# Kernel tuning notes

Measured on AMD Instinct MI355X. Metric: run time of the kernel, lower is better.

Reference implementation:

```python
import math
import jax, jax.numpy as jnp
import numpy as np

D_MODEL = 2048
HEAD = 128
DEPTH = 12
LAMBDA_INIT = 0.8 - 0.6 * math.exp(-0.3 * DEPTH)
RMS_EPS = float(np.finfo(np.float32).eps)  # torch RMSNorm default eps=None -> finfo.eps


def setup_inputs() -> dict:
    key = jax.random.key(0)
    ks = jax.random.split(key, 9)
    B, S = 2, 4096
    std_l = 0.1
    return {
        "x": jax.random.normal(ks[0], (B, S, D_MODEL), dtype=jnp.float32),
        "Wq": jax.random.normal(ks[1], (HEAD, D_MODEL), dtype=jnp.float32) / math.sqrt(D_MODEL),
        "Wk": jax.random.normal(ks[2], (HEAD, D_MODEL), dtype=jnp.float32) / math.sqrt(D_MODEL),
        "Wv": jax.random.normal(ks[3], (HEAD, D_MODEL), dtype=jnp.float32) / math.sqrt(D_MODEL),
        "lambda_q1": std_l * jax.random.normal(ks[4], (HEAD // 2,), dtype=jnp.float32),
        "lambda_q2": std_l * jax.random.normal(ks[5], (HEAD // 2,), dtype=jnp.float32),
        "lambda_k1": std_l * jax.random.normal(ks[6], (HEAD // 2,), dtype=jnp.float32),
        "lambda_k2": std_l * jax.random.normal(ks[7], (HEAD // 2,), dtype=jnp.float32),
        "rms_weight": jnp.ones((HEAD,), dtype=jnp.float32),
    }


def reference(x, Wq, Wk, Wv, lambda_q1, lambda_q2, lambda_k1, lambda_k2, rms_weight):
    # projections (torch Linear: x @ W.T)
    q = jnp.einsum("bsd,hd->bsh", x, Wq)
    k = jnp.einsum("bsd,hd->bsh", x, Wk)
    v = jnp.einsum("bsd,hd->bsh", x, Wv)
    h2 = HEAD // 2
    q1, q2 = q[..., :h2], q[..., h2:]
    k1, k2 = k[..., :h2], k[..., h2:]
    scale = 1.0 / math.sqrt(h2)
    attn1 = jax.nn.softmax(jnp.einsum("bqh,bkh->bqk", q1, k1) * scale, axis=-1)
    attn2 = jax.nn.softmax(jnp.einsum("bqh,bkh->bqk", q2, k2) * scale, axis=-1)
    lam = jnp.exp(jnp.dot(lambda_q1, lambda_k1)) - jnp.exp(jnp.dot(lambda_q2, lambda_k2)) + LAMBDA_INIT
    attn_out = jnp.einsum("bqk,bkh->bqh", attn1 - lam * attn2, v)
    # RMSNorm over last dim
    rms = jax.lax.rsqrt(jnp.mean(attn_out * attn_out, axis=-1, keepdims=True) + RMS_EPS)
    return (1.0 - LAMBDA_INIT) * (attn_out * rms * rms_weight)
```

## Files before the change

kernel.cpp:

```cpp
#include <hip/hip_runtime.h>
#include <hip/hip_bf16.h>
#include <math.h>

#define S_LEN 4096
#define DMODEL 2048
#define HEADD 128

typedef __attribute__((ext_vector_type(8))) short short8;
typedef __attribute__((ext_vector_type(4))) float floatx4;

__device__ __forceinline__ short f2bs(float f) {
  __hip_bfloat16 h = __float2bfloat16(f);
  short s; __builtin_memcpy(&s, &h, 2); return s;
}
__device__ __forceinline__ float bs2f(short s) {
  unsigned u = ((unsigned)(unsigned short)s) << 16;
  float f; __builtin_memcpy(&f, &u, 4); return f;
}
__device__ __forceinline__ int pkbf(float a, float b) {
  return (int)(((unsigned)(unsigned short)f2bs(b) << 16) |
               (unsigned)(unsigned short)f2bs(a));
}
__device__ __forceinline__ float fexp2(float x) { return __builtin_amdgcn_exp2f(x); }

__global__ __launch_bounds__(256) void convw_kernel(const float* __restrict__ wq,
                                                    const float* __restrict__ wk,
                                                    const float* __restrict__ wv,
                                                    short* __restrict__ wc) {
  const int per = 128 * 2048;
  int e = (blockIdx.x * blockDim.x + threadIdx.x) * 4;
  const float* src = (e < per) ? wq : (e < 2 * per) ? wk : wv;
  int off = e & (per - 1);
  float4 v = *(const float4*)(src + off);
  short4 r;
  r.x = f2bs(v.x); r.y = f2bs(v.y); r.z = f2bs(v.z); r.w = f2bs(v.w);
  *(short4*)(wc + e) = r;
}

__global__ __launch_bounds__(256, 3) void proj_kernel(const float* __restrict__ x,
                                                      const short* __restrict__ wc,
                                                      short* __restrict__ qm,
                                                      short* __restrict__ kb,
                                                      short* __restrict__ vstage) {
  const int tid = threadIdx.x;
  const int w = tid >> 6;
  const int lane = tid & 63;
  const int lo = lane & 15, g = lane >> 4;
  const int id = blockIdx.x;
  const int nq = id >> 7, mb = id & 127;
  const int m0 = mb * 64;
  const int n0 = nq * 96;

  __shared__ short xt[2][64 * 64];
  __shared__ short wt[2][96 * 64];

  const int r8 = tid >> 3, sc = tid & 7;
  const float* xs0 = x + (size_t)(m0 + r8) * DMODEL + sc * 8;
  const float* xs1 = x + (size_t)(m0 + 32 + r8) * DMODEL + sc * 8;
  const short* ws0 = wc + (size_t)(n0 + r8) * DMODEL + sc * 8;
  const short* ws1 = wc + (size_t)(n0 + 32 + r8) * DMODEL + sc * 8;
  const short* ws2 = wc + (size_t)(n0 + 64 + r8) * DMODEL + sc * 8;
  const int xl0 = r8 * 64 + ((sc ^ (r8 & 7)) * 8);
  const int xl1 = (32 + r8) * 64 + ((sc ^ (r8 & 7)) * 8);
  const int wlo0 = r8 * 64 + ((sc ^ (r8 & 7)) * 8);
  const int wlo1 = (32 + r8) * 64 + ((sc ^ (r8 & 7)) * 8);
  const int wlo2 = (64 + r8) * 64 + ((sc ^ (r8 & 7)) * 8);

  const int mrow = (w >> 1) * 32;
  const int ncol = (w & 1) * 48;
  int aoff[2][2], boff[3][2];
#pragma unroll
  for (int mi = 0; mi < 2; ++mi) {
    int r = mrow + mi * 16 + lo;
#pragma unroll
    for (int kc = 0; kc < 2; ++kc)
      aoff[mi][kc] = r * 64 + (((kc * 4 + g) ^ (r & 7)) * 8);
  }
#pragma unroll
  for (int t = 0; t < 3; ++t) {
    int r = ncol + t * 16 + lo;
#pragma unroll
    for (int kc = 0; kc < 2; ++kc)
      boff[t][kc] = r * 64 + (((kc * 4 + g) ^ (r & 7)) * 8);
  }

  floatx4 acc[2][3];
#pragma unroll
  for (int mi = 0; mi < 2; ++mi)
#pragma unroll
    for (int t = 0; t < 3; ++t) acc[mi][t] = floatx4{0.f, 0.f, 0.f, 0.f};

  {
    float4 a0 = *(const float4*)(xs0), a1 = *(const float4*)(xs0 + 4);
    float4 b0 = *(const float4*)(xs1), b1 = *(const float4*)(xs1 + 4);
    int4 w0 = *(const int4*)(ws0);
    int4 w1 = *(const int4*)(ws1);
    int4 w2 = *(const int4*)(ws2);
    short8 sA, sB;
    sA[0]=f2bs(a0.x); sA[1]=f2bs(a0.y); sA[2]=f2bs(a0.z); sA[3]=f2bs(a0.w);
    sA[4]=f2bs(a1.x); sA[5]=f2bs(a1.y); sA[6]=f2bs(a1.z); sA[7]=f2bs(a1.w);
    sB[0]=f2bs(b0.x); sB[1]=f2bs(b0.y); sB[2]=f2bs(b0.z); sB[3]=f2bs(b0.w);
    sB[4]=f2bs(b1.x); sB[5]=f2bs(b1.y); sB[6]=f2bs(b1.z); sB[7]=f2bs(b1.w);
    *(short8*)&xt[0][xl0] = sA;
    *(short8*)&xt[0][xl1] = sB;
    *(int4*)&wt[0][wlo0] = w0;
    *(int4*)&wt[0][wlo1] = w1;
    *(int4*)&wt[0][wlo2] = w2;
  }
  __syncthreads();

  int cur = 0;
#pragma unroll 1
  for (int it = 0; it < 32; ++it) {
    float4 a0, a1, b0, b1;
    int4 w0, w1, w2;
    if (it + 1 < 32) {
      const int k = (it + 1) * 64;
      a0 = *(const float4*)(xs0 + k); a1 = *(const float4*)(xs0 + k + 4);
      b0 = *(const float4*)(xs1 + k); b1 = *(const float4*)(xs1 + k + 4);
      w0 = *(const int4*)(ws0 + k);
      w1 = *(const int4*)(ws1 + k);
      w2 = *(const int4*)(ws2 + k);
    }

    {
      const short* xb = &xt[cur][0];
      const short* wb = &wt[cur][0];
      short8 af[2][2], bf[3][2];
#pragma unroll
      for (int mi = 0; mi < 2; ++mi)
#pragma unroll
        for (int kc = 0; kc < 2; ++kc) af[mi][kc] = *(const short8*)(xb + aoff[mi][kc]);
#pragma unroll
      for (int t = 0; t < 3; ++t)
#pragma unroll
        for (int kc = 0; kc < 2; ++kc) bf[t][kc] = *(const short8*)(wb + boff[t][kc]);
#pragma unroll
      for (int kc = 0; kc < 2; ++kc)
#pragma unroll
        for (int mi = 0; mi < 2; ++mi)
#pragma unroll
          for (int t = 0; t < 3; ++t)
            acc[mi][t] = __builtin_amdgcn_mfma_f32_16x16x32_bf16(af[mi][kc], bf[t][kc], acc[mi][t], 0, 0, 0);
    }

    if (it + 1 < 32) {
      short8 sA, sB;
      sA[0]=f2bs(a0.x); sA[1]=f2bs(a0.y); sA[2]=f2bs(a0.z); sA[3]=f2bs(a0.w);
      sA[4]=f2bs(a1.x); sA[5]=f2bs(a1.y); sA[6]=f2bs(a1.z); sA[7]=f2bs(a1.w);
      sB[0]=f2bs(b0.x); sB[1]=f2bs(b0.y); sB[2]=f2bs(b0.z); sB[3]=f2bs(b0.w);
      sB[4]=f2bs(b1.x); sB[5]=f2bs(b1.y); sB[6]=f2bs(b1.z); sB[7]=f2bs(b1.w);
      *(short8*)&xt[cur ^ 1][xl0] = sA;
      *(short8*)&xt[cur ^ 1][xl1] = sB;
      *(int4*)&wt[cur ^ 1][wlo0] = w0;
      *(int4*)&wt[cur ^ 1][wlo1] = w1;
      *(int4*)&wt[cur ^ 1][wlo2] = w2;
    }
    __syncthreads();
    cur ^= 1;
  }

#pragma unroll
  for (int t = 0; t < 3; ++t) {
    int n = n0 + ncol + t * 16 + lo;
#pragma unroll
    for (int mi = 0; mi < 2; ++mi)
#pragma unroll
      for (int j = 0; j < 4; ++j) {
        int m = m0 + mrow + mi * 16 + g * 4 + j;
        float v = acc[mi][t][j];
        if (n < HEADD) {
          qm[(size_t)m * HEADD + n] = f2bs(v * 0.18033688011112042f);
        } else if (n < 2 * HEADD) {
          kb[(size_t)m * HEADD + (n - HEADD)] = f2bs(v);
        } else {
          vstage[(size_t)m * HEADD + (n - 2 * HEADD)] = f2bs(v);
        }
      }
  }
}

__global__ __launch_bounds__(256) void conv_v_kernel(const short* __restrict__ vstage,
                                                     short* __restrict__ vt) {
  const int tid = threadIdx.x;
  const int bb = blockIdx.x >> 6, st = blockIdx.x & 63;
  const int s0 = st * 64;

  __shared__ short ld[64][136];

  const int r = tid >> 2, c8 = (tid & 3) * 32;
#pragma unroll
  for (int q = 0; q < 4; ++q) {
    const size_t off = (size_t)(bb * 4096 + s0 + r) * 128 + c8 + q * 8;
    *(short8*)(&ld[r][c8 + q * 8]) = *(const short8*)(vstage + off);
  }
  __syncthreads();

  const int h = tid >> 1, sh = (tid & 1) * 32;
#pragma unroll
  for (int q = 0; q < 4; ++q) {
    short8 t;
#pragma unroll
    for (int i = 0; i < 8; ++i) {
      int src5 = (i < 4) ? (4 * q + i) : (16 + 4 * q + (i - 4));
      t[i] = ld[sh + src5][h];
    }
    *(short8*)(vt + ((size_t)bb * 128 + h) * 4096 + s0 + sh + q * 8) = t;
  }
}

__global__ __launch_bounds__(256, 3) void attn_kernel(const short* __restrict__ qm,
                                                      const short* __restrict__ kb,
                                                      const short* __restrict__ vt,
                                                      short* __restrict__ po,
                                                      float* __restrict__ pls) {
  const int tid = threadIdx.x;
  const int w = tid >> 6;
  const int lane = tid & 63;
  const int lo = lane & 15, g = lane >> 4;
  const int qsp = w >> 1;
  const int s = w & 1;
  const int id = blockIdx.x;
  const int ksp = id & 7;
  const int qblk = id >> 3;
  const int b = qblk >> 6;
  const int kv_base = ksp * 512;

  __shared__ short kt[2][32 * 128];
  __shared__ short vl[2][128 * 32];

  const int kr0 = tid >> 4, kck = tid & 15;
  const int vr0 = tid >> 2, vck = tid & 3;
  const short* kS = kb + (size_t)b * S_LEN * HEADD;
  const short* vS = vt + (size_t)b * HEADD * S_LEN;
  const int kld0 = kr0 * 128 + ((kck ^ (kr0 & 7)) * 8);
  const int kld1 = (kr0 + 16) * 128 + ((kck ^ (kr0 & 7)) * 8);
  const int vld0 = vr0 * 32 + ((vck ^ (vr0 & 3)) * 8);
  const int vld1 = (vr0 + 64) * 32 + ((vck ^ (vr0 & 3)) * 8);

  const int rowqA = qblk * 64 + qsp * 32;
  const int rowqB = rowqA + 16;
  const short* qrowA = qm + (size_t)(rowqA + lo) * HEADD + s * 64;
  const short* qrowB = qm + (size_t)(rowqB + lo) * HEADD + s * 64;
  const short8 qA0 = *(const short8*)(qrowA + g * 8);
  const short8 qA1 = *(const short8*)(qrowA + 32 + g * 8);
  const short8 qB0 = *(const short8*)(qrowB + g * 8);
  const short8 qB1 = *(const short8*)(qrowB + 32 + g * 8);

  floatx4 accA[8], accB[8];
#pragma unroll
  for (int n = 0; n < 8; ++n) {
    accA[n] = floatx4{0.f, 0.f, 0.f, 0.f};
    accB[n] = floatx4{0.f, 0.f, 0.f, 0.f};
  }
  float lxA = 0.f, lxB = 0.f;

  const int kc0 = ((s * 8 + g) ^ (lo & 7)) * 8;
  const int kc1 = ((s * 8 + 4 + g) ^ (lo & 7)) * 8;
  const int kro0 = lo * 128, kro1 = (16 + lo) * 128;
  const int vco = (g ^ (lo & 3)) * 8;

  {
    int4 ka = *(const int4*)(kS + (size_t)(kv_base + kr0) * HEADD + kck * 8);
    int4 kbx = *(const int4*)(kS + (size_t)(kv_base + kr0 + 16) * HEADD + kck * 8);
    int4 va = *(const int4*)(vS + (size_t)vr0 * S_LEN + kv_base + vck * 8);
    int4 vb = *(const int4*)(vS + (size_t)(vr0 + 64) * S_LEN + kv_base + vck * 8);
    *(int4*)(&kt[0][kld0]) = ka;
    *(int4*)(&kt[0][kld1]) = kbx;
    *(int4*)(&vl[0][vld0]) = va;
    *(int4*)(&vl[0][vld1]) = vb;
  }
  __syncthreads();

  int cur = 0;
#pragma unroll 1
  for (int it = 0; it < 16; ++it) {
    int4 ka, kbx, va, vb;
    if (it + 1 < 16) {
      const int kvn = kv_base + (it + 1) * 32;
      ka  = *(const int4*)(kS + (size_t)(kvn + kr0) * HEADD + kck * 8);
      kbx = *(const int4*)(kS + (size_t)(kvn + kr0 + 16) * HEADD + kck * 8);
      va  = *(const int4*)(vS + (size_t)vr0 * S_LEN + kvn + vck * 8);
      vb  = *(const int4*)(vS + (size_t)(vr0 + 64) * S_LEN + kvn + vck * 8);
    }

    const short* kbase = &kt[cur][0];
    short8 a00 = *(const short8*)(kbase + kro0 + kc0);
    short8 a01 = *(const short8*)(kbase + kro0 + kc1);
    short8 a10 = *(const short8*)(kbase + kro1 + kc0);
    short8 a11 = *(const short8*)(kbase + kro1 + kc1);

    floatx4 z = floatx4{0.f, 0.f, 0.f, 0.f};
    floatx4 u;
    u = __builtin_amdgcn_mfma_f32_16x16x32_bf16(a00, qA0, z, 0, 0, 0);
    floatx4 T0A = __builtin_amdgcn_mfma_f32_16x16x32_bf16(a01, qA1, u, 0, 0, 0);
    u = __builtin_amdgcn_mfma_f32_16x16x32_bf16(a10, qA0, z, 0, 0, 0);
    floatx4 T1A = __builtin_amdgcn_mfma_f32_16x16x32_bf16(a11, qA1, u, 0, 0, 0);
    u = __builtin_amdgcn_mfma_f32_16x16x32_bf16(a00, qB0, z, 0, 0, 0);
    floatx4 T0B = __builtin_amdgcn_mfma_f32_16x16x32_bf16(a01, qB1, u, 0, 0, 0);
    u = __builtin_amdgcn_mfma_f32_16x16x32_bf16(a10, qB0, z, 0, 0, 0);
    floatx4 T1B = __builtin_amdgcn_mfma_f32_16x16x32_bf16(a11, qB1, u, 0, 0, 0);

    short8 paA, paB;
    {
      float p0 = fexp2(T0A[0]), p1 = fexp2(T0A[1]), p2 = fexp2(T0A[2]), p3 = fexp2(T0A[3]);
      float p4 = fexp2(T1A[0]), p5 = fexp2(T1A[1]), p6 = fexp2(T1A[2]), p7 = fexp2(T1A[3]);
      float lp = ((p0 + p1) + (p2 + p3)) + ((p4 + p5) + (p6 + p7));
      lp += __shfl_xor(lp, 16);
      lp += __shfl_xor(lp, 32);
      lxA += lp;
      int4 tmp = {pkbf(p0, p1), pkbf(p2, p3), pkbf(p4, p5), pkbf(p6, p7)};
      __builtin_memcpy(&paA, &tmp, 16);
    }
    {
      float p0 = fexp2(T0B[0]), p1 = fexp2(T0B[1]), p2 = fexp2(T0B[2]), p3 = fexp2(T0B[3]);
      float p4 = fexp2(T1B[0]), p5 = fexp2(T1B[1]), p6 = fexp2(T1B[2]), p7 = fexp2(T1B[3]);
      float lp = ((p0 + p1) + (p2 + p3)) + ((p4 + p5) + (p6 + p7));
      lp += __shfl_xor(lp, 16);
      lp += __shfl_xor(lp, 32);
      lxB += lp;
      int4 tmp = {pkbf(p0, p1), pkbf(p2, p3), pkbf(p4, p5), pkbf(p6, p7)};
      __builtin_memcpy(&paB, &tmp, 16);
    }

    const short* vbase = &vl[cur][0];
#pragma unroll
    for (int n = 0; n < 8; ++n) {
      short8 vf = *(const short8*)(vbase + (n * 16 + lo) * 32 + vco);
      accA[n] = __builtin_amdgcn_mfma_f32_16x16x32_bf16(paA, vf, accA[n], 0, 0, 0);
      accB[n] = __builtin_amdgcn_mfma_f32_16x16x32_bf16(paB, vf, accB[n], 0, 0, 0);
    }

    if (it + 1 < 16) {
      *(int4*)(&kt[cur ^ 1][kld0]) = ka;
      *(int4*)(&kt[cur ^ 1][kld1]) = kbx;
      *(int4*)(&vl[cur ^ 1][vld0]) = va;
      *(int4*)(&vl[cur ^ 1][vld1]) = vb;
    }
    __syncthreads();
    cur ^= 1;
  }

  short* pw = po + ((size_t)(ksp * 2 + s) * 8192) * 128;
#pragma unroll
  for (int j = 0; j < 4; ++j) {
    short8 pk;
#pragma unroll
    for (int n = 0; n < 8; ++n) pk[n] = f2bs(accA[n][j]);
    *(short8*)(pw + (size_t)(rowqA + g * 4 + j) * 128 + lo * 8) = pk;
#pragma unroll
    for (int n = 0; n < 8; ++n) pk[n] = f2bs(accB[n][j]);
    *(short8*)(pw + (size_t)(rowqB + g * 4 + j) * 128 + lo * 8) = pk;
  }
  if (g == 0) {
    pls[(size_t)(ksp * 2 + s) * 8192 + rowqA + lo] = lxA;
    pls[(size_t)(ksp * 2 + s) * 8192 + rowqB + lo] = lxB;
  }
}

__global__ __launch_bounds__(256) void merge_kernel(const short* __restrict__ po,
                                                    const float* __restrict__ pls,
                                                    const float* __restrict__ lq1,
                                                    const float* __restrict__ lq2,
                                                    const float* __restrict__ lk1,
                                                    const float* __restrict__ lk2,
                                                    const float* __restrict__ rmsw,
                                                    float* __restrict__ out) {
  const int tid = threadIdx.x;
  const int row = blockIdx.x * 16 + (tid >> 4);
  const int lo = tid & 15;

  float a1s = 0.f, a2s = 0.f;
  for (int i = 0; i < 64; ++i) {
    a1s = fmaf(lq1[i], lk1[i], a1s);
    a2s = fmaf(lq2[i], lk2[i], a2s);
  }
  const float lam = __expf(a1s) - __expf(a2s) + 0.7836057665316245f;

  float o1[8], o2[8];
#pragma unroll
  for (int n = 0; n < 8; ++n) { o1[n] = 0.f; o2[n] = 0.f; }
  float l1 = 0.f, l2 = 0.f;
#pragma unroll
  for (int ksp = 0; ksp < 8; ++ksp) {
    short8 sa = *(const short8*)(po + ((size_t)(ksp * 2 + 0) * 8192 + row) * 128 + lo * 8);
    short8 sb = *(const short8*)(po + ((size_t)(ksp * 2 + 1) * 8192 + row) * 128 + lo * 8);
#pragma unroll
    for (int n = 0; n < 8; ++n) { o1[n] += bs2f(sa[n]); o2[n] += bs2f(sb[n]); }
    l1 += pls[(size_t)(ksp * 2 + 0) * 8192 + row];
    l2 += pls[(size_t)(ksp * 2 + 1) * 8192 + row];
  }
  const float iL1 = 1.f / l1, iL2 = 1.f / l2;

  float v[8];
  float ssq = 0.f;
#pragma unroll
  for (int n = 0; n < 8; ++n) {
    v[n] = o1[n] * iL1 - lam * (o2[n] * iL2);
    ssq += v[n] * v[n];
  }
  ssq += __shfl_xor(ssq, 1);
  ssq += __shfl_xor(ssq, 2);
  ssq += __shfl_xor(ssq, 4);
  ssq += __shfl_xor(ssq, 8);
  const float rr = rsqrtf(ssq * (1.f / 128.f) + 1.1920928955078125e-07f);

  float* ob = out + (size_t)row * 128;
#pragma unroll
  for (int n = 0; n < 8; ++n) {
    int c = n * 16 + lo;
    ob[c] = 0.21639423346837554f * v[n] * rr * rmsw[c];
  }
}

extern "C" void kernel_launch(void* const* d_in, const int* in_sizes, int n_in,
                              void* d_out, int out_size, void* d_ws, size_t ws_size,
                              hipStream_t stream) {
  const float* x   = (const float*)d_in[0];
  const float* wq  = (const float*)d_in[1];
  const float* wk  = (const float*)d_in[2];
  const float* wv  = (const float*)d_in[3];
  const float* lq1 = (const float*)d_in[4];
  const float* lq2 = (const float*)d_in[5];
  const float* lk1 = (const float*)d_in[6];
  const float* lk2 = (const float*)d_in[7];
  const float* rw  = (const float*)d_in[8];
  float* out = (float*)d_out;

  char* ws = (char*)d_ws;
  short* qm  = (short*)(ws);
  short* kb  = (short*)(ws + (2u << 20));
  short* vt  = (short*)(ws + (4u << 20));
  short* wc  = (short*)(ws + (6u << 20));
  short* vstage = (short*)(ws + (6u << 20) + 1572864u);
  short* po  = (short*)(ws + (8u << 20));
  float* pls = (float*)(ws + (40u << 20));

  convw_kernel<<<768, 256, 0, stream>>>(wq, wk, wv, wc);
  proj_kernel<<<512, 256, 0, stream>>>(x, wc, qm, kb, vstage);
  conv_v_kernel<<<128, 256, 0, stream>>>(vstage, vt);
  attn_kernel<<<1024, 256, 0, stream>>>(qm, kb, vt, po, pls);
  merge_kernel<<<512, 256, 0, stream>>>(po, pls, lq1, lq2, lk1, lk2, rw, out);
}
```

Before: 92.73 us.

## Split projection GEMM along K into two halves with a reduction pass

The projection kernel now splits the 2048-long reduction into two halves across twice as many blocks, writing bf16 partial results to two staging buffers. A new conv_qk kernel sums the partials, applies the Q scale and writes Q and K, and the V transpose kernel now also sums its two partials. The aim is to raise occupancy and parallelism on a 512-block GEMM that underfills the GPU, at the cost of an extra launch, extra global traffic, and rounding partial sums to bf16 before they are added.

Measured after the change: 92.07 us. Within noise of the previous version (-0.7%).

```diff
diff --git a/kernel.cpp b/kernel.cpp
--- a/kernel.cpp
+++ b/kernel.cpp
@@ -39,27 +39,28 @@
 
 __global__ __launch_bounds__(256, 3) void proj_kernel(const float* __restrict__ x,
                                                       const short* __restrict__ wc,
-                                                      short* __restrict__ qm,
-                                                      short* __restrict__ kb,
-                                                      short* __restrict__ vstage) {
+                                                      short* __restrict__ qa0,
+                                                      short* __restrict__ qa1) {
   const int tid = threadIdx.x;
   const int w = tid >> 6;
   const int lane = tid & 63;
   const int lo = lane & 15, g = lane >> 4;
   const int id = blockIdx.x;
-  const int nq = id >> 7, mb = id & 127;
+  const int kh = id >> 9, nq = (id >> 7) & 3, mb = id & 127;
   const int m0 = mb * 64;
   const int n0 = nq * 96;
+  const int k0 = kh * 1024;
+  short* qa = kh ? qa1 : qa0;
 
   __shared__ short xt[2][64 * 64];
   __shared__ short wt[2][96 * 64];
 
   const int r8 = tid >> 3, sc = tid & 7;
-  const float* xs0 = x + (size_t)(m0 + r8) * DMODEL + sc * 8;
-  const float* xs1 = x + (size_t)(m0 + 32 + r8) * DMODEL + sc * 8;
-  const short* ws0 = wc + (size_t)(n0 + r8) * DMODEL + sc * 8;
-  const short* ws1 = wc + (size_t)(n0 + 32 + r8) * DMODEL + sc * 8;
-  const short* ws2 = wc + (size_t)(n0 + 64 + r8) * DMODEL + sc * 8;
+  const float* xs0 = x + (size_t)(m0 + r8) * DMODEL + k0 + sc * 8;
+  const float* xs1 = x + (size_t)(m0 + 32 + r8) * DMODEL + k0 + sc * 8;
+  const short* ws0 = wc + (size_t)(n0 + r8) * DMODEL + k0 + sc * 8;
+  const short* ws1 = wc + (size_t)(n0 + 32 + r8) * DMODEL + k0 + sc * 8;
+  const short* ws2 = wc + (size_t)(n0 + 64 + r8) * DMODEL + k0 + sc * 8;
   const int xl0 = r8 * 64 + ((sc ^ (r8 & 7)) * 8);
   const int xl1 = (32 + r8) * 64 + ((sc ^ (r8 & 7)) * 8);
   const int wlo0 = r8 * 64 + ((sc ^ (r8 & 7)) * 8);
@@ -111,10 +112,10 @@
 
   int cur = 0;
 #pragma unroll 1
-  for (int it = 0; it < 32; ++it) {
+  for (int it = 0; it < 16; ++it) {
     float4 a0, a1, b0, b1;
     int4 w0, w1, w2;
-    if (it + 1 < 32) {
+    if (it + 1 < 16) {
       const int k = (it + 1) * 64;
       a0 = *(const float4*)(xs0 + k); a1 = *(const float4*)(xs0 + k + 4);
       b0 = *(const float4*)(xs1 + k); b1 = *(const float4*)(xs1 + k + 4);
@@ -144,7 +145,7 @@
             acc[mi][t] = __builtin_amdgcn_mfma_f32_16x16x32_bf16(af[mi][kc], bf[t][kc], acc[mi][t], 0, 0, 0);
     }
 
-    if (it + 1 < 32) {
+    if (it + 1 < 16) {
       short8 sA, sB;
       sA[0]=f2bs(a0.x); sA[1]=f2bs(a0.y); sA[2]=f2bs(a0.z); sA[3]=f2bs(a0.w);
       sA[4]=f2bs(a1.x); sA[5]=f2bs(a1.y); sA[6]=f2bs(a1.z); sA[7]=f2bs(a1.w);
@@ -168,19 +169,37 @@
 #pragma unroll
       for (int j = 0; j < 4; ++j) {
         int m = m0 + mrow + mi * 16 + g * 4 + j;
-        float v = acc[mi][t][j];
-        if (n < HEADD) {
-          qm[(size_t)m * HEADD + n] = f2bs(v * 0.18033688011112042f);
-        } else if (n < 2 * HEADD) {
-          kb[(size_t)m * HEADD + (n - HEADD)] = f2bs(v);
-        } else {
-          vstage[(size_t)m * HEADD + (n - 2 * HEADD)] = f2bs(v);
-        }
+        qa[(size_t)m * 384 + n] = f2bs(acc[mi][t][j]);
       }
   }
 }
 
-__global__ __launch_bounds__(256) void conv_v_kernel(const short* __restrict__ vstage,
+__global__ __launch_bounds__(256) void conv_qk_kernel(const short* __restrict__ qa0,
+                                                      const short* __restrict__ qa1,
+                                                      short* __restrict__ qm,
+                                                      short* __restrict__ kb) {
+  int e = (blockIdx.x * 256 + threadIdx.x) * 4;
+  int m = e >> 8, c = e & 255;
+  short4 a = *(const short4*)(qa0 + (size_t)m * 384 + c);
+  short4 b = *(const short4*)(qa1 + (size_t)m * 384 + c);
+  float vx = bs2f(a.x) + bs2f(b.x);
+  float vy = bs2f(a.y) + bs2f(b.y);
+  float vz = bs2f(a.z) + bs2f(b.z);
+  float vw = bs2f(a.w) + bs2f(b.w);
+  short4 r;
+  if (c < 128) {
+    const float sc = 0.18033688011112042f;
+    r.x = f2bs(vx * sc); r.y = f2bs(vy * sc);
+    r.z = f2bs(vz * sc); r.w = f2bs(vw * sc);
+    *(short4*)(qm + (size_t)m * 128 + c) = r;
+  } else {
+    r.x = f2bs(vx); r.y = f2bs(vy); r.z = f2bs(vz); r.w = f2bs(vw);
+    *(short4*)(kb + (size_t)m * 128 + (c - 128)) = r;
+  }
+}
+
+__global__ __launch_bounds__(256) void conv_v_kernel(const short* __restrict__ qa0,
+                                                     const short* __restrict__ qa1,
                                                      short* __restrict__ vt) {
   const int tid = threadIdx.x;
   const int bb = blockIdx.x >> 6, st = blockIdx.x & 63;
@@ -191,8 +210,13 @@
   const int r = tid >> 2, c8 = (tid & 3) * 32;
 #pragma unroll
   for (int q = 0; q < 4; ++q) {
-    const size_t off = (size_t)(bb * 4096 + s0 + r) * 128 + c8 + q * 8;
-    *(short8*)(&ld[r][c8 + q * 8]) = *(const short8*)(vstage + off);
+    const size_t off = (size_t)(bb * 4096 + s0 + r) * 384 + 256 + c8 + q * 8;
+    short8 a = *(const short8*)(qa0 + off);
+    short8 b = *(const short8*)(qa1 + off);
+    short8 o;
+#pragma unroll
+    for (int i = 0; i < 8; ++i) o[i] = f2bs(bs2f(a[i]) + bs2f(b[i]));
+    *(short8*)(&ld[r][c8 + q * 8]) = o;
   }
   __syncthreads();
 
@@ -432,13 +456,15 @@
   short* kb  = (short*)(ws + (2u << 20));
   short* vt  = (short*)(ws + (4u << 20));
   short* wc  = (short*)(ws + (6u << 20));
-  short* vstage = (short*)(ws + (6u << 20) + 1572864u);
+  short* qa0 = (short*)(ws + (8u << 20));
+  short* qa1 = (short*)(ws + (8u << 20) + 6291456u);
   short* po  = (short*)(ws + (8u << 20));
   float* pls = (float*)(ws + (40u << 20));
 
   convw_kernel<<<768, 256, 0, stream>>>(wq, wk, wv, wc);
-  proj_kernel<<<512, 256, 0, stream>>>(x, wc, qm, kb, vstage);
-  conv_v_kernel<<<128, 256, 0, stream>>>(vstage, vt);
+  proj_kernel<<<1024, 256, 0, stream>>>(x, wc, qa0, qa1);
+  conv_qk_kernel<<<2048, 256, 0, stream>>>(qa0, qa1, qm, kb);
+  conv_v_kernel<<<128, 256, 0, stream>>>(qa0, qa1, vt);
   attn_kernel<<<1024, 256, 0, stream>>>(qm, kb, vt, po, pls);
   merge_kernel<<<512, 256, 0, stream>>>(po, pls, lq1, lq2, lk1, lk2, rw, out);
 }
```
